# Kernel optimization log

Hardware: AMD Instinct MI355X
Metric: run time of the kernel (lower is better)

## Reference

```python
import jax, jax.numpy as jnp
import numpy as np

B, SQ, SK, D = 8, 2048, 2048, 256

def setup_inputs() -> dict:
    key = jax.random.key(0)
    ks = jax.random.split(key, 8)
    x1 = jax.random.normal(ks[0], (B, SQ, D), dtype=jnp.float32)
    x2 = jax.random.normal(ks[1], (B, SK, D), dtype=jnp.float32)
    x3 = jax.random.normal(ks[2], (B, SK, D), dtype=jnp.float32)  # unused by the original forward (value=x3 is dead)
    mask = jax.random.bernoulli(ks[3], 0.8, (B, SK))
    scale = 0.02
    Wq = jax.random.normal(ks[4], (D, D), dtype=jnp.float32) * scale
    Wk = jax.random.normal(ks[5], (D, D), dtype=jnp.float32) * scale
    Wv = jax.random.normal(ks[6], (D, D), dtype=jnp.float32) * scale
    bq = jnp.zeros((D,), jnp.float32)
    bk = jnp.zeros((D,), jnp.float32)
    bv = jnp.zeros((D,), jnp.float32)
    return {"x1": x1, "x2": x2, "x3": x3, "Wq": Wq, "Wk": Wk, "Wv": Wv,
            "bq": bq, "bk": bk, "bv": bv, "mask": mask}

def reference(x1, x2, x3, Wq, Wk, Wv, bq, bk, bv, mask):
    d = x1.shape[-1]
    inv_sqrt_d = 1.0 / jnp.sqrt(jnp.asarray(d, x1.dtype))
    # Projections (single-head MHA with query scaling, as in torch MHA internals)
    q = (x1 @ Wq + bq) * inv_sqrt_d          # [B, SQ, D]
    k = x2 @ Wk + bk                          # [B, SK, D]
    v = x2 @ Wv + bv                          # forward_value(key): value projected from key input
    # Raw scores
    qk = jnp.einsum('bqd,bkd->bqk', q, k)     # [B, SQ, SK]
    # Mask-derived per-column rescale: qk /= (mask.size(0)/mask.sum(-2))**0.5
    m = mask.astype(qk.dtype)                 # [B, SK]
    col_count = jnp.sum(m, axis=0, keepdims=True)           # [1, SK]
    factor = jnp.sqrt(jnp.asarray(mask.shape[0], qk.dtype) / col_count)  # [1, SK]
    qk = qk / factor                          # broadcast over [B, SQ, SK]; div-by-inf -> 0 where column count is 0
    attn = jax.nn.softmax(qk, axis=-1)
    # dropout is identity in eval / p=0
    out = jnp.einsum('bqk,bkd->bqd', attn, v)  # [B, SQ, D]
    return out
```

## Files before the change

### kernel.cpp

```cpp
#include <hip/hip_runtime.h>
#include <hip/hip_bf16.h>
#include <math.h>

#define B_  8
#define SQ_ 2048
#define SK_ 2048
#define D_  256
#define NSPLIT 4
#define KEYS_PER_SPLIT (SK_ / NSPLIT)
#define NT (KEYS_PER_SPLIT / 32)

typedef __attribute__((ext_vector_type(8))) short bf16x8;
typedef __attribute__((ext_vector_type(4))) float f32x4;
typedef __attribute__((ext_vector_type(4))) unsigned short u16x4;
typedef __attribute__((ext_vector_type(8))) _Float16 f16x8;
typedef __attribute__((ext_vector_type(4))) _Float16 f16x4;
typedef __attribute__((ext_vector_type(4))) unsigned int u32x4;

static __device__ __forceinline__ unsigned short f2bf(float f) {
    unsigned int u = __builtin_bit_cast(unsigned int, f);
    u += 0x7FFFu + ((u >> 16) & 1u);
    return (unsigned short)(u >> 16);
}

static __device__ __forceinline__ void gld_lds16(const unsigned short* g, unsigned short* l) {
    __builtin_amdgcn_global_load_lds(
        (const __attribute__((address_space(1))) unsigned int*)g,
        (__attribute__((address_space(3))) unsigned int*)l, 16, 0, 0);
}

#define VMCNT(n)  asm volatile("s_waitcnt vmcnt(" #n ")" ::: "memory")
#define LGKM0_SB  do { asm volatile("s_waitcnt lgkmcnt(0)" ::: "memory"); \
                       __builtin_amdgcn_sched_barrier(0); } while (0)

__global__ void prep_kernel(const float* __restrict__ Wq, const float* __restrict__ Wk,
                            const float* __restrict__ Wv, const int* __restrict__ mask,
                            unsigned short* __restrict__ wP, float* __restrict__ r) {
    int bid = blockIdx.x, tid = threadIdx.x;
    if (bid < 96) {
        int p = bid >> 5, c = (bid >> 2) & 7, it = bid & 3;
        const float* W = (p == 0 ? Wq : (p == 1 ? Wk : Wv));
        int chunk = it * 256 + tid;
        int nt = chunk >> 6, lane = chunk & 63;
        int l15 = lane & 15, quad = lane >> 4;
        int n = nt * 16 + l15;
        unsigned short* dst = wP + (size_t)(((p * 8 + c) * 16 + nt) * 1024 + lane * 8);
#pragma unroll
        for (int j = 0; j < 8; j++)
            dst[j] = f2bf(W[(size_t)(c * 32 + quad * 8 + j) * D_ + n]);
    } else {
        int s = (bid - 96) * 256 + tid;
        float c = 0.f;
#pragma unroll
        for (int b = 0; b < B_; b++) c += (mask[b * SK_ + s] != 0) ? 1.f : 0.f;
        r[s] = sqrtf(c * 0.125f);
    }
}

__global__ __launch_bounds__(256) void proj_kernel(
    const float* __restrict__ x1, const float* __restrict__ x2,
    const float* __restrict__ bq, const float* __restrict__ bk, const float* __restrict__ bv,
    const unsigned short* __restrict__ wP, const float* __restrict__ r,
    unsigned short* __restrict__ qb, unsigned short* __restrict__ kP,
    unsigned short* __restrict__ vP)
{
    __shared__ unsigned short sbuf[18432];
    const int tid = threadIdx.x;
    const int wv = tid >> 6, lane = tid & 63, l15 = lane & 15, quad = lane >> 4;
    const int mt = blockIdx.x, b = blockIdx.y, p = blockIdx.z;
    const int s0w = mt * 64 + wv * 16;

    const float* x = (p == 0 ? x1 : x2) + ((size_t)b * SQ_ + s0w + l15) * D_;
    const unsigned short* wbase = wP + (size_t)(p * 8) * 16 * 1024;
    const float* bias = (p == 0 ? bq : (p == 1 ? bk : bv));

    auto stage = [&](int c) {
        const unsigned short* src = wbase + (size_t)c * 16384;
        unsigned short* dst = sbuf + (c & 1) * 8192;
#pragma unroll
        for (int i = 0; i < 4; i++) {
            int nt = i * 4 + wv;
            gld_lds16(src + nt * 1024 + lane * 8, dst + (i * 4 + wv) * 512);
        }
    };
    stage(0);

    float4 xa[8], xb[8];
#pragma unroll
    for (int c = 0; c < 8; c++) {
        xa[c] = *(const float4*)(x + c * 32 + quad * 8);
        xb[c] = *(const float4*)(x + c * 32 + quad * 8 + 4);
    }
    bf16x8 af[8];
#pragma unroll
    for (int c = 0; c < 8; c++) {
        bf16x8 t;
        t[0] = (short)f2bf(xa[c].x); t[1] = (short)f2bf(xa[c].y);
        t[2] = (short)f2bf(xa[c].z); t[3] = (short)f2bf(xa[c].w);
        t[4] = (short)f2bf(xb[c].x); t[5] = (short)f2bf(xb[c].y);
        t[6] = (short)f2bf(xb[c].z); t[7] = (short)f2bf(xb[c].w);
        af[c] = t;
    }

    float bb[16];
#pragma unroll
    for (int nt = 0; nt < 16; nt++) bb[nt] = bias[nt * 16 + l15];

    f32x4 acc[16];
#pragma unroll
    for (int n = 0; n < 16; n++) acc[n] = (f32x4){0.f, 0.f, 0.f, 0.f};

    for (int c = 0; c < 8; c++) {
        __syncthreads();
        if (c + 1 < 8) stage(c + 1);
        const unsigned short* lb = sbuf + (c & 1) * 8192 + lane * 8;
#pragma unroll
        for (int nt = 0; nt < 16; nt++) {
            bf16x8 wf = *(const bf16x8*)(lb + nt * 512);
            acc[nt] = __builtin_amdgcn_mfma_f32_16x16x32_bf16(af[c], wf, acc[nt], 0, 0, 0);
        }
    }
    __syncthreads();

    if (p == 2) {
#pragma unroll
        for (int nt = 0; nt < 16; nt++) {
            int d = nt * 16 + l15;
            u16x4 u;
#pragma unroll
            for (int g = 0; g < 4; g++) u[g] = f2bf(acc[nt][g] + bb[nt]);
            *(u16x4*)(sbuf + (size_t)d * 72 + wv * 16 + quad * 4) = u;
        }
        __syncthreads();
#pragma unroll
        for (int it = 0; it < 8; it++) {
            int chunk = it * 256 + tid;
            int tt = chunk >> 10, n = (chunk >> 6) & 15, ln = chunk & 63;
            bf16x8 v = *(const bf16x8*)(sbuf + (size_t)(n * 16 + (ln & 15)) * 72 + tt * 32 + (ln >> 4) * 8);
            *(bf16x8*)(vP + (((size_t)(b * 64 + mt * 2 + tt) * 16 + n) * 512) + ln * 8) = v;
        }
    } else if (p == 0) {
        float rv = 0.0625f;
        unsigned short* my = sbuf + wv * 2176;
#pragma unroll
        for (int h = 0; h < 2; h++) {
#pragma unroll
            for (int nt8 = 0; nt8 < 8; nt8++) {
                int nt = h * 8 + nt8;
#pragma unroll
                for (int g = 0; g < 4; g++) {
                    float v = (acc[nt][g] + bb[nt]) * rv;
                    my[(quad * 4 + g) * 136 + nt8 * 16 + l15] = f2bf(v);
                }
            }
            asm volatile("s_waitcnt lgkmcnt(0)" ::: "memory");
#pragma unroll
            for (int i2 = 0; i2 < 4; i2++) {
                int row = i2 * 4 + quad;
                bf16x8 v = *(const bf16x8*)(my + row * 136 + l15 * 8);
                *(bf16x8*)(qb + ((size_t)(b * SQ_ + s0w + row)) * D_ + h * 128 + l15 * 8) = v;
            }
        }
    } else {
        const int t = mt * 2 + (wv >> 1), hfrag = wv & 1;
        float rv[4];
#pragma unroll
        for (int g = 0; g < 4; g++) rv[g] = r[s0w + quad * 4 + g];
        unsigned short* my = sbuf + wv * 2176;
#pragma unroll
        for (int hp = 0; hp < 2; hp++) {
#pragma unroll
            for (int nt8 = 0; nt8 < 8; nt8++) {
                int nt = hp * 8 + nt8;
#pragma unroll
                for (int g = 0; g < 4; g++) {
                    float v = (acc[nt][g] + bb[nt]) * rv[g];
                    my[(quad * 4 + g) * 136 + nt8 * 16 + l15] = f2bf(v);
                }
            }
            asm volatile("s_waitcnt lgkmcnt(0)" ::: "memory");
#pragma unroll
            for (int cc = 0; cc < 4; cc++) {
                bf16x8 v = *(const bf16x8*)(my + (size_t)l15 * 136 + cc * 32 + quad * 8);
                *(bf16x8*)(kP + ((((size_t)(b * 64 + t) * 2 + hfrag) * 8 + hp * 4 + cc) * 512) + lane * 8) = v;
            }
        }
    }
}

__global__ __launch_bounds__(256, 2) void flash_kernel(
    const unsigned short* __restrict__ qb, const unsigned short* __restrict__ kP,
    const unsigned short* __restrict__ vP, _Float16* __restrict__ Op,
    float* __restrict__ lp)
{
    __shared__ unsigned short Ks[2][16 * 512];
    __shared__ unsigned short Vs[2][16 * 512];
    const int tid = threadIdx.x;
    const int wv = tid >> 6, lane = tid & 63, l15 = lane & 15, quad = lane >> 4;
    const int bid = blockIdx.x;
    const int g = bid & 31, q = bid >> 5;
    const int b = g >> 2, sp = g & 3;
    const int q0 = q * 128 + wv * 32;

    const unsigned short* kpb = kP + (size_t)(b * 64 + sp * 16) * 8192;
    const unsigned short* vpb = vP + (size_t)(b * 64 + sp * 16) * 8192;

    const int c0 = tid * 8;

#pragma unroll
    for (int i = 0; i < 4; i++)
        gld_lds16(kpb + (size_t)i * 2048 + c0, &Ks[0][i * 2048 + wv * 512]);
#pragma unroll
    for (int i = 0; i < 4; i++)
        gld_lds16(vpb + (size_t)i * 2048 + c0, &Vs[0][i * 2048 + wv * 512]);

    bf16x8 qf[2][8];
#pragma unroll
    for (int mt = 0; mt < 2; mt++) {
        const unsigned short* qrow = qb + ((size_t)(b * SQ_ + q0 + mt * 16 + l15)) * D_;
#pragma unroll
        for (int c = 0; c < 8; c++)
            qf[mt][c] = *(const bf16x8*)(qrow + c * 32 + quad * 8);
    }

    f32x4 o[2][16];
#pragma unroll
    for (int mt = 0; mt < 2; mt++)
#pragma unroll
        for (int n = 0; n < 16; n++) o[mt][n] = (f32x4){0.f, 0.f, 0.f, 0.f};
    float l_[2] = {0.f, 0.f};

    const unsigned short* kfr = &Ks[0][0] + lane * 8;
    const unsigned short* vfr = &Vs[0][0] + lane * 8;

    for (int kt = 0; kt < NT; kt++) {
        const int cur = kt & 1;
        const unsigned short* kc = kfr + cur * (16 * 512);
        const unsigned short* vc = vfr + cur * (16 * 512);
        const bool pre = (kt + 1 < NT);

        VMCNT(4);
        bf16x8 kf0[8];
#pragma unroll
        for (int c = 0; c < 8; c++) kf0[c] = *(const bf16x8*)(kc + c * 512);
        if (pre) {
            const unsigned short* kn = kpb + (size_t)(kt + 1) * 8192;
#pragma unroll
            for (int i = 0; i < 4; i++)
                gld_lds16(kn + (size_t)i * 2048 + c0, &Ks[cur ^ 1][i * 2048 + wv * 512]);
        }
        __builtin_amdgcn_s_barrier();
        LGKM0_SB;
        f32x4 s[2][2];
        s[0][0] = (f32x4){0.f,0.f,0.f,0.f}; s[0][1] = (f32x4){0.f,0.f,0.f,0.f};
        s[1][0] = (f32x4){0.f,0.f,0.f,0.f}; s[1][1] = (f32x4){0.f,0.f,0.f,0.f};
        __builtin_amdgcn_s_setprio(1);
#pragma unroll
        for (int c = 0; c < 8; c++) {
            s[0][0] = __builtin_amdgcn_mfma_f32_16x16x32_bf16(kf0[c], qf[0][c], s[0][0], 0, 0, 0);
            s[1][0] = __builtin_amdgcn_mfma_f32_16x16x32_bf16(kf0[c], qf[1][c], s[1][0], 0, 0, 0);
        }
        __builtin_amdgcn_s_setprio(0);

        bf16x8 kf1[8];
#pragma unroll
        for (int c = 0; c < 8; c++) kf1[c] = *(const bf16x8*)(kc + (8 + c) * 512);
        if (pre) {
            const unsigned short* vn = vpb + (size_t)(kt + 1) * 8192;
#pragma unroll
            for (int i = 0; i < 4; i++)
                gld_lds16(vn + (size_t)i * 2048 + c0, &Vs[cur ^ 1][i * 2048 + wv * 512]);
        }
        __builtin_amdgcn_s_barrier();
        LGKM0_SB;
        __builtin_amdgcn_s_setprio(1);
#pragma unroll
        for (int c = 0; c < 8; c++) {
            s[0][1] = __builtin_amdgcn_mfma_f32_16x16x32_bf16(kf1[c], qf[0][c], s[0][1], 0, 0, 0);
            s[1][1] = __builtin_amdgcn_mfma_f32_16x16x32_bf16(kf1[c], qf[1][c], s[1][1], 0, 0, 0);
        }
        __builtin_amdgcn_s_setprio(0);

        bf16x8 pf[2];
#pragma unroll
        for (int mt = 0; mt < 2; mt++) {
            float e0 = __expf(s[mt][0][0]), e1 = __expf(s[mt][0][1]);
            float e2 = __expf(s[mt][0][2]), e3 = __expf(s[mt][0][3]);
            float f0 = __expf(s[mt][1][0]), f1 = __expf(s[mt][1][1]);
            float f2 = __expf(s[mt][1][2]), f3 = __expf(s[mt][1][3]);
            l_[mt] += (e0 + e1 + e2 + e3) + (f0 + f1 + f2 + f3);
            unsigned int pk0, pk1, pk2, pk3;
            asm("v_cvt_pk_bf16_f32 %0, %1, %2" : "=v"(pk0) : "v"(e0), "v"(e1));
            asm("v_cvt_pk_bf16_f32 %0, %1, %2" : "=v"(pk1) : "v"(e2), "v"(e3));
            asm("v_cvt_pk_bf16_f32 %0, %1, %2" : "=v"(pk2) : "v"(f0), "v"(f1));
            asm("v_cvt_pk_bf16_f32 %0, %1, %2" : "=v"(pk3) : "v"(f2), "v"(f3));
            asm("v_permlane32_swap_b32 %0, %1" : "+v"(pk0), "+v"(pk2));
            asm("v_permlane16_swap_b32 %0, %1" : "+v"(pk0), "+v"(pk2));
            asm("v_permlane32_swap_b32 %0, %1" : "+v"(pk1), "+v"(pk3));
            asm("v_permlane16_swap_b32 %0, %1" : "+v"(pk1), "+v"(pk3));
            u32x4 w = (u32x4){pk0, pk1, pk2, pk3};
            pf[mt] = __builtin_bit_cast(bf16x8, w);
        }

        if (pre) { VMCNT(8); }
        else     { VMCNT(0); }
        bf16x8 vf0[8];
#pragma unroll
        for (int n = 0; n < 8; n++) vf0[n] = *(const bf16x8*)(vc + n * 512);
        __builtin_amdgcn_s_barrier();
        LGKM0_SB;
        __builtin_amdgcn_s_setprio(1);
#pragma unroll
        for (int n = 0; n < 8; n++) {
            o[0][n] = __builtin_amdgcn_mfma_f32_16x16x32_bf16(vf0[n], pf[0], o[0][n], 0, 0, 0);
            o[1][n] = __builtin_amdgcn_mfma_f32_16x16x32_bf16(vf0[n], pf[1], o[1][n], 0, 0, 0);
        }
        __builtin_amdgcn_s_setprio(0);

        bf16x8 vf1[8];
#pragma unroll
        for (int n = 0; n < 8; n++) vf1[n] = *(const bf16x8*)(vc + (8 + n) * 512);
        __builtin_amdgcn_s_barrier();
        LGKM0_SB;
        __builtin_amdgcn_s_setprio(1);
#pragma unroll
        for (int n = 0; n < 8; n++) {
            o[0][8 + n] = __builtin_amdgcn_mfma_f32_16x16x32_bf16(vf1[n], pf[0], o[0][8 + n], 0, 0, 0);
            o[1][8 + n] = __builtin_amdgcn_mfma_f32_16x16x32_bf16(vf1[n], pf[1], o[1][8 + n], 0, 0, 0);
        }
        __builtin_amdgcn_s_setprio(0);
    }

#pragma unroll
    for (int mt = 0; mt < 2; mt++) {
        float t = l_[mt];
        t += __shfl_xor(t, 16, 64);
        t += __shfl_xor(t, 32, 64);
        l_[mt] = t;
    }

    _Float16* op = Op + ((size_t)(sp * B_ + b) * SQ_ + q0) * D_;
#pragma unroll
    for (int mt = 0; mt < 2; mt++) {
        _Float16* rowp = op + (size_t)(mt * 16 + l15) * D_ + quad * 4;
#pragma unroll
        for (int n = 0; n < 16; n++) {
            f16x4 v4;
#pragma unroll
            for (int g2 = 0; g2 < 4; g2++) v4[g2] = (_Float16)(o[mt][n][g2]);
            *(f16x4*)(rowp + n * 16) = v4;
        }
    }
    if (quad == 0) {
        float* lpp = lp + (size_t)(sp * B_ + b) * SQ_ + q0;
        lpp[l15] = l_[0];
        lpp[16 + l15] = l_[1];
    }
}

__global__ __launch_bounds__(256) void combine_kernel(
    const _Float16* __restrict__ Op, const float* __restrict__ lp,
    float* __restrict__ out)
{
    const int gid = blockIdx.x * 256 + threadIdx.x;
    const int row = gid >> 5;
    const size_t base = (size_t)gid * 8;
    float l = lp[row] + lp[B_ * SQ_ + row] + lp[2 * B_ * SQ_ + row] + lp[3 * B_ * SQ_ + row];
    float inv = 1.f / l;
    float acc[8] = {0,0,0,0,0,0,0,0};
#pragma unroll
    for (int sp = 0; sp < NSPLIT; sp++) {
        f16x8 v = *(const f16x8*)(Op + (size_t)sp * B_ * SQ_ * D_ + base);
#pragma unroll
        for (int j = 0; j < 8; j++) acc[j] += (float)v[j];
    }
    float4 r0 = {acc[0] * inv, acc[1] * inv, acc[2] * inv, acc[3] * inv};
    float4 r1 = {acc[4] * inv, acc[5] * inv, acc[6] * inv, acc[7] * inv};
    *(float4*)(out + base) = r0;
    *(float4*)(out + base + 4) = r1;
}

extern "C" void kernel_launch(void* const* d_in, const int* in_sizes, int n_in,
                              void* d_out, int out_size, void* d_ws, size_t ws_size,
                              hipStream_t stream)
{
    const float* x1 = (const float*)d_in[0];
    const float* x2 = (const float*)d_in[1];
    const float* Wq = (const float*)d_in[3];
    const float* Wk = (const float*)d_in[4];
    const float* Wv = (const float*)d_in[5];
    const float* bq = (const float*)d_in[6];
    const float* bk = (const float*)d_in[7];
    const float* bv = (const float*)d_in[8];
    const int*  mask = (const int*)d_in[9];
    float* out = (float*)d_out;

    char* ws = (char*)d_ws;
    unsigned short* qb = (unsigned short*)(ws);
    unsigned short* kP = (unsigned short*)(ws + 8388608);
    unsigned short* vP = (unsigned short*)(ws + 16777216);
    float*          r  = (float*)(ws + 25165824);
    float*          lp = (float*)(ws + 25174016);
    _Float16*       Op = (_Float16*)(ws + 25436160);
    unsigned short* wP = (unsigned short*)(ws + 25436160);

    prep_kernel<<<dim3(96 + SK_ / 256), 256, 0, stream>>>(Wq, Wk, Wv, mask, wP, r);
    proj_kernel<<<dim3(SQ_ / 64, B_, 3), 256, 0, stream>>>(x1, x2, bq, bk, bv, wP, r, qb, kP, vP);
    flash_kernel<<<dim3((SQ_ / 128) * B_ * NSPLIT), 256, 0, stream>>>(qb, kP, vP, Op, lp);
    combine_kernel<<<dim3((B_ * SQ_ * D_ / 8) / 256), 256, 0, stream>>>(Op, lp, out);
}
```

Before: 169.5 us.

## Double projection row tile per block to reuse staged weight fragments

The projection kernel now gives each wave 32 rows (two 16-row MFMA tiles) instead of 16, so each block covers 128 rows and the grid halves. Each weight fragment read from LDS feeds two MFMAs, which halves weight staging traffic and barrier count per row. The cost is more registers (twice the accumulators and A fragments), handled with a launch bound of 2 blocks per CU, plus a two-phase LDS transpose for the V output. The K and V packed layout indexing is remapped to match.

Measured after the change: 184.3 us. 8.7% more time.

```diff
diff --git a/kernel.cpp b/kernel.cpp
--- a/kernel.cpp
+++ b/kernel.cpp
@@ -57,7 +57,7 @@
     }
 }
 
-__global__ __launch_bounds__(256) void proj_kernel(
+__global__ __launch_bounds__(256, 2) void proj_kernel(
     const float* __restrict__ x1, const float* __restrict__ x2,
     const float* __restrict__ bq, const float* __restrict__ bk, const float* __restrict__ bv,
     const unsigned short* __restrict__ wP, const float* __restrict__ r,
@@ -67,10 +67,11 @@
     __shared__ unsigned short sbuf[18432];
     const int tid = threadIdx.x;
     const int wv = tid >> 6, lane = tid & 63, l15 = lane & 15, quad = lane >> 4;
-    const int mt = blockIdx.x, b = blockIdx.y, p = blockIdx.z;
-    const int s0w = mt * 64 + wv * 16;
-
-    const float* x = (p == 0 ? x1 : x2) + ((size_t)b * SQ_ + s0w + l15) * D_;
+    const int blk = blockIdx.x, b = blockIdx.y, p = blockIdx.z;
+    const int s0 = blk * 128;
+    const int s0w = s0 + wv * 32;
+
+    const float* xsrc = (p == 0 ? x1 : x2) + (size_t)b * SQ_ * D_;
     const unsigned short* wbase = wP + (size_t)(p * 8) * 16 * 1024;
     const float* bias = (p == 0 ? bq : (p == 1 ? bk : bv));
 
@@ -80,35 +81,37 @@
 #pragma unroll
         for (int i = 0; i < 4; i++) {
             int nt = i * 4 + wv;
-            gld_lds16(src + nt * 1024 + lane * 8, dst + (i * 4 + wv) * 512);
+            gld_lds16(src + nt * 1024 + lane * 8, dst + nt * 512);
         }
     };
     stage(0);
 
-    float4 xa[8], xb[8];
-#pragma unroll
-    for (int c = 0; c < 8; c++) {
-        xa[c] = *(const float4*)(x + c * 32 + quad * 8);
-        xb[c] = *(const float4*)(x + c * 32 + quad * 8 + 4);
-    }
-    bf16x8 af[8];
-#pragma unroll
-    for (int c = 0; c < 8; c++) {
-        bf16x8 t;
-        t[0] = (short)f2bf(xa[c].x); t[1] = (short)f2bf(xa[c].y);
-        t[2] = (short)f2bf(xa[c].z); t[3] = (short)f2bf(xa[c].w);
-        t[4] = (short)f2bf(xb[c].x); t[5] = (short)f2bf(xb[c].y);
-        t[6] = (short)f2bf(xb[c].z); t[7] = (short)f2bf(xb[c].w);
-        af[c] = t;
+    bf16x8 af[2][8];
+#pragma unroll
+    for (int mt = 0; mt < 2; mt++) {
+        const float* x = xsrc + (size_t)(s0w + mt * 16 + l15) * D_;
+#pragma unroll
+        for (int c = 0; c < 8; c++) {
+            float4 a0 = *(const float4*)(x + c * 32 + quad * 8);
+            float4 a1 = *(const float4*)(x + c * 32 + quad * 8 + 4);
+            bf16x8 t;
+            t[0] = (short)f2bf(a0.x); t[1] = (short)f2bf(a0.y);
+            t[2] = (short)f2bf(a0.z); t[3] = (short)f2bf(a0.w);
+            t[4] = (short)f2bf(a1.x); t[5] = (short)f2bf(a1.y);
+            t[6] = (short)f2bf(a1.z); t[7] = (short)f2bf(a1.w);
+            af[mt][c] = t;
+        }
     }
 
     float bb[16];
 #pragma unroll
     for (int nt = 0; nt < 16; nt++) bb[nt] = bias[nt * 16 + l15];
 
-    f32x4 acc[16];
-#pragma unroll
-    for (int n = 0; n < 16; n++) acc[n] = (f32x4){0.f, 0.f, 0.f, 0.f};
+    f32x4 acc[2][16];
+#pragma unroll
+    for (int mt = 0; mt < 2; mt++)
+#pragma unroll
+        for (int n = 0; n < 16; n++) acc[mt][n] = (f32x4){0.f, 0.f, 0.f, 0.f};
 
     for (int c = 0; c < 8; c++) {
         __syncthreads();
@@ -117,72 +120,90 @@
 #pragma unroll
         for (int nt = 0; nt < 16; nt++) {
             bf16x8 wf = *(const bf16x8*)(lb + nt * 512);
-            acc[nt] = __builtin_amdgcn_mfma_f32_16x16x32_bf16(af[c], wf, acc[nt], 0, 0, 0);
+            acc[0][nt] = __builtin_amdgcn_mfma_f32_16x16x32_bf16(af[0][c], wf, acc[0][nt], 0, 0, 0);
+            acc[1][nt] = __builtin_amdgcn_mfma_f32_16x16x32_bf16(af[1][c], wf, acc[1][nt], 0, 0, 0);
         }
     }
     __syncthreads();
 
     if (p == 2) {
 #pragma unroll
-        for (int nt = 0; nt < 16; nt++) {
-            int d = nt * 16 + l15;
-            u16x4 u;
-#pragma unroll
-            for (int g = 0; g < 4; g++) u[g] = f2bf(acc[nt][g] + bb[nt]);
-            *(u16x4*)(sbuf + (size_t)d * 72 + wv * 16 + quad * 4) = u;
-        }
-        __syncthreads();
-#pragma unroll
-        for (int it = 0; it < 8; it++) {
-            int chunk = it * 256 + tid;
-            int tt = chunk >> 10, n = (chunk >> 6) & 15, ln = chunk & 63;
-            bf16x8 v = *(const bf16x8*)(sbuf + (size_t)(n * 16 + (ln & 15)) * 72 + tt * 32 + (ln >> 4) * 8);
-            *(bf16x8*)(vP + (((size_t)(b * 64 + mt * 2 + tt) * 16 + n) * 512) + ln * 8) = v;
+        for (int hh = 0; hh < 2; hh++) {
+            if ((wv >> 1) == hh) {
+                int scol = (wv & 1) * 32;
+#pragma unroll
+                for (int mt = 0; mt < 2; mt++)
+#pragma unroll
+                    for (int nt = 0; nt < 16; nt++) {
+                        int d = nt * 16 + l15;
+                        u16x4 u;
+#pragma unroll
+                        for (int g = 0; g < 4; g++) u[g] = f2bf(acc[mt][nt][g] + bb[nt]);
+                        *(u16x4*)(sbuf + (size_t)d * 72 + scol + mt * 16 + quad * 4) = u;
+                    }
+            }
+            __syncthreads();
+#pragma unroll
+            for (int it = 0; it < 8; it++) {
+                int chunk = it * 256 + tid;
+                int tt = chunk >> 10, n = (chunk >> 6) & 15, ln = chunk & 63;
+                bf16x8 v = *(const bf16x8*)(sbuf + (size_t)(n * 16 + (ln & 15)) * 72 + tt * 32 + (ln >> 4) * 8);
+                *(bf16x8*)(vP + (((size_t)(b * 64 + blk * 4 + hh * 2 + tt) * 16 + n) * 512) + ln * 8) = v;
+            }
+            if (hh == 0) __syncthreads();
         }
     } else if (p == 0) {
         float rv = 0.0625f;
         unsigned short* my = sbuf + wv * 2176;
 #pragma unroll
-        for (int h = 0; h < 2; h++) {
-#pragma unroll
-            for (int nt8 = 0; nt8 < 8; nt8++) {
-                int nt = h * 8 + nt8;
-#pragma unroll
-                for (int g = 0; g < 4; g++) {
-                    float v = (acc[nt][g] + bb[nt]) * rv;
-                    my[(quad * 4 + g) * 136 + nt8 * 16 + l15] = f2bf(v);
+        for (int mt = 0; mt < 2; mt++) {
+#pragma unroll
+            for (int h = 0; h < 2; h++) {
+#pragma unroll
+                for (int nt8 = 0; nt8 < 8; nt8++) {
+                    int nt = h * 8 + nt8;
+#pragma unroll
+                    for (int g = 0; g < 4; g++) {
+                        float v = (acc[mt][nt][g] + bb[nt]) * rv;
+                        my[(quad * 4 + g) * 136 + nt8 * 16 + l15] = f2bf(v);
+                    }
+                }
+                asm volatile("s_waitcnt lgkmcnt(0)" ::: "memory");
+#pragma unroll
+                for (int i2 = 0; i2 < 4; i2++) {
+                    int row = i2 * 4 + quad;
+                    bf16x8 v = *(const bf16x8*)(my + row * 136 + l15 * 8);
+                    *(bf16x8*)(qb + ((size_t)(b * SQ_ + s0w + mt * 16 + row)) * D_ + h * 128 + l15 * 8) = v;
                 }
             }
-            asm volatile("s_waitcnt lgkmcnt(0)" ::: "memory");
-#pragma unroll
-            for (int i2 = 0; i2 < 4; i2++) {
-                int row = i2 * 4 + quad;
-                bf16x8 v = *(const bf16x8*)(my + row * 136 + l15 * 8);
-                *(bf16x8*)(qb + ((size_t)(b * SQ_ + s0w + row)) * D_ + h * 128 + l15 * 8) = v;
-            }
         }
     } else {
-        const int t = mt * 2 + (wv >> 1), hfrag = wv & 1;
-        float rv[4];
-#pragma unroll
-        for (int g = 0; g < 4; g++) rv[g] = r[s0w + quad * 4 + g];
+        const int t = blk * 4 + wv;
+        float rv[2][4];
+#pragma unroll
+        for (int mt = 0; mt < 2; mt++)
+#pragma unroll
+            for (int g = 0; g < 4; g++) rv[mt][g] = r[s0w + mt * 16 + quad * 4 + g];
         unsigned short* my = sbuf + wv * 2176;
 #pragma unroll
-        for (int hp = 0; hp < 2; hp++) {
-#pragma unroll
-            for (int nt8 = 0; nt8 < 8; nt8++) {
-                int nt = hp * 8 + nt8;
-#pragma unroll
-                for (int g = 0; g < 4; g++) {
-                    float v = (acc[nt][g] + bb[nt]) * rv[g];
-                    my[(quad * 4 + g) * 136 + nt8 * 16 + l15] = f2bf(v);
+        for (int mt = 0; mt < 2; mt++) {
+#pragma unroll
+            for (int hp = 0; hp < 2; hp++) {
+#pragma unroll
+                for (int nt8 = 0; nt8 < 8; nt8++) {
+                    int nt = hp * 8 + nt8;
+#pragma unroll
+                    for (int g = 0; g < 4; g++) {
+                        float v = (acc[mt][nt][g] + bb[nt]) * rv[mt][g];
+                        my[(quad * 4 + g) * 136 + nt8 * 16 + l15] = f2bf(v);
+                    }
                 }
-            }
-            asm volatile("s_waitcnt lgkmcnt(0)" ::: "memory");
-#pragma unroll
-            for (int cc = 0; cc < 4; cc++) {
-                bf16x8 v = *(const bf16x8*)(my + (size_t)l15 * 136 + cc * 32 + quad * 8);
-                *(bf16x8*)(kP + ((((size_t)(b * 64 + t) * 2 + hfrag) * 8 + hp * 4 + cc) * 512) + lane * 8) = v;
+                asm volatile("s_waitcnt lgkmcnt(0)" ::: "memory");
+#pragma unroll
+                for (int cc = 0; cc < 4; cc++) {
+                    bf16x8 v = *(const bf16x8*)(my + (size_t)l15 * 136 + cc * 32 + quad * 8);
+                    *(bf16x8*)(kP + ((((size_t)(b * 64 + t) * 2 + mt) * 8 + hp * 4 + cc) * 512) + lane * 8) = v;
+                }
             }
         }
     }
@@ -405,7 +426,7 @@
     unsigned short* wP = (unsigned short*)(ws + 25436160);
 
     prep_kernel<<<dim3(96 + SK_ / 256), 256, 0, stream>>>(Wq, Wk, Wv, mask, wP, r);
-    proj_kernel<<<dim3(SQ_ / 64, B_, 3), 256, 0, stream>>>(x1, x2, bq, bk, bv, wP, r, qb, kP, vP);
+    proj_kernel<<<dim3(SQ_ / 128, B_, 3), 256, 0, stream>>>(x1, x2, bq, bk, bv, wP, r, qb, kP, vP);
     flash_kernel<<<dim3((SQ_ / 128) * B_ * NSPLIT), 256, 0, stream>>>(qb, kP, vP, Op, lp);
     combine_kernel<<<dim3((B_ * SQ_ * D_ / 8) / 256), 256, 0, stream>>>(Op, lp, out);
 }
```
